# Performance work log

Measured on AMD Instinct MI355X. Metric: run time of the kernel, lower is better.

The kernel has to match this reference:

```python
import jax, jax.numpy as jnp
import numpy as np

SCORE_THR = 0.01
IOU_THR = 0.1          # NOTE: original layer hardcodes 0.1 in tf.image.non_max_suppression
MAX_DET = 100
NEG = jnp.float32(-1e30)


def _iou_one_vs_all(box, boxes):
    # box: [4] (y1,x1,y2,x2), boxes: [N,4]
    y1 = jnp.maximum(box[0], boxes[:, 0])
    x1 = jnp.maximum(box[1], boxes[:, 1])
    y2 = jnp.minimum(box[2], boxes[:, 2])
    x2 = jnp.minimum(box[3], boxes[:, 3])
    inter = jnp.maximum(y2 - y1, 0.0) * jnp.maximum(x2 - x1, 0.0)
    a = (box[2] - box[0]) * (box[3] - box[1])
    b = (boxes[:, 2] - boxes[:, 0]) * (boxes[:, 3] - boxes[:, 1])
    return inter / (a + b - inter + 1e-8)


def _nms_keep(boxes, scores):
    # Greedy NMS as a keep-mask over N anchors. Matches tf.image.non_max_suppression
    # restricted to anchors with score > SCORE_THR, up to MAX_DET selections.
    s = jnp.where(scores > SCORE_THR, scores, NEG)
    keep0 = jnp.zeros(s.shape, dtype=bool)

    def step(carry, _):
        s, keep = carry
        i = jnp.argmax(s)
        ok = s[i] > NEG * 0.5
        keep = keep.at[i].set(ok)
        iou = _iou_one_vs_all(boxes[i], boxes)
        s = jnp.where((iou > IOU_THR) & ok, NEG, s)
        s = s.at[i].set(NEG)
        return (s, keep), None

    (_, keep), _ = jax.lax.scan(step, (s, keep0), None, length=MAX_DET)
    return keep


def _filter_image(boxes_i, cls_i):
    # boxes_i: [N,4], cls_i: [N,C]
    C = cls_i.shape[1]
    # class-specific NMS: keep mask per class -> [C, N]
    keep = jax.vmap(lambda s: _nms_keep(boxes_i, s))(cls_i.T)
    keep_flat = keep.T.reshape(-1)          # [N*C], (anchor, class) flat order
    flat = cls_i.reshape(-1)                # [N*C]
    masked = jnp.where(keep_flat, flat, NEG)
    vals, idx = jax.lax.top_k(masked, MAX_DET)
    valid = vals > NEG * 0.5
    anchor = idx // C
    label = idx % C
    scores_out = jnp.where(valid, jnp.take(flat, idx), -1.0)
    boxes_out = jnp.where(valid[:, None], boxes_i[anchor], -1.0)
    labels_out = jnp.where(valid, label, -1).astype(jnp.int32)
    return boxes_out, scores_out, labels_out


def setup_inputs() -> dict:
    key = jax.random.key(0)
    k1, k2, k3 = jax.random.split(key, 3)
    B, N, C = 4, 49104, 90
    yx1 = jax.random.uniform(k1, (B, N, 2), dtype=jnp.float32) * 512.0
    hw = jax.random.uniform(k2, (B, N, 2), dtype=jnp.float32) * 128.0 + 1.0
    boxes = jnp.concatenate([yx1, yx1 + hw], axis=-1)          # [B,N,4] y1x1y2x2
    classification = jax.random.uniform(k3, (B, N, C), dtype=jnp.float32)
    return {"boxes": boxes, "classification": classification}


def reference(boxes, classification):
    return jax.vmap(_filter_image)(boxes, classification)
```

## Files before the change

kernel.cpp:

```cpp
#include <hip/hip_runtime.h>
#include <stdint.h>

typedef unsigned long long u64;

#define B_ 4
#define N_ 49104
#define C_ 90
#define NCLS (B_ * C_)
#define MAXK 100
#define THR 0.01f
#define NBH 288
#define BINLO 1760
#define KCAP 640
#define PTGT 448
#define PCAP 512
#define ACH 128
#define NCH ((N_ + ACH - 1) / ACH)
#define CAPC 32
#define NBIN_M 1280
#define BINBASE 0x3F6E0000u
#define BINSH_M 10
#define T0 0.99f

__device__ __forceinline__ float area_of(float y1, float x1, float y2, float x2) {
#pragma clang fp contract(off)
  return (y2 - y1) * (x2 - x1);
}

#define IOU_MID (26843547.0 / 268435456.0)

__device__ __forceinline__ bool iou_gt(float ay1, float ax1, float ay2, float ax2, float aa,
                                       float by1, float bx1, float by2, float bx2, float ba) {
#pragma clang fp contract(off)
  float y1 = fmaxf(ay1, by1);
  float x1 = fmaxf(ax1, bx1);
  float y2 = fminf(ay2, by2);
  float x2 = fminf(ax2, bx2);
  float inter = fmaxf(y2 - y1, 0.0f) * fmaxf(x2 - x1, 0.0f);
  float denom = aa + ba - inter + 1e-8f;
  return (double)inter >= IOU_MID * (double)denom;
}

__device__ __forceinline__ u64 umax64(u64 a, u64 b) { return a > b ? a : b; }

__device__ __forceinline__ u64 shfl_xor_u64(u64 v, int m) {
  int lo = __shfl_xor((int)(unsigned)v, m);
  int hi = __shfl_xor((int)(unsigned)(v >> 32), m);
  return ((u64)(unsigned)hi << 32) | (u64)(unsigned)lo;
}

__device__ __forceinline__ int key2bin_m(u64 k) {
  int d = (int)((unsigned)(k >> 32) - BINBASE);
  int bin = d >> BINSH_M;
  if (d < 0) bin = 0;
  if (bin > NBIN_M - 1) bin = NBIN_M - 1;
  return bin;
}

__device__ __forceinline__ int keybin_h(u64 k) {
  int bin = (int)((unsigned)(k >> 44) & 2047) - BINLO;
  if (bin < 0) bin = 0;
  if (bin > NBH - 1) bin = NBH - 1;
  return bin;
}

__global__ __launch_bounds__(256) void select_kernel(const float* __restrict__ cls,
                                                     u64* __restrict__ keybuf,
                                                     unsigned* __restrict__ cnt,
                                                     int capsel, float t0) {
  __shared__ u64 ll[C_ * CAPC];
  __shared__ unsigned lcnt[C_];
  __shared__ unsigned base_s[C_];
  int blk = blockIdx.x;
  int b = blk / NCH, ch = blk - b * NCH;
  int a0 = ch * ACH;
  int aEnd = a0 + ACH; if (aEnd > N_) aEnd = N_;
  int e0 = a0 * C_;
  int nelem = (aEnd - a0) * C_;
  int tid = threadIdx.x;

  for (int i = tid; i < C_; i += 256) lcnt[i] = 0u;
  __syncthreads();

  const float4* src4 = (const float4*)(cls + (size_t)b * N_ * C_ + e0);
  int n4 = nelem >> 2;
  for (int i4 = tid; i4 < n4; i4 += 256) {
    float4 v = src4[i4];
#pragma unroll
    for (int j = 0; j < 4; ++j) {
      float s = (&v.x)[j];
      if (s > t0) {
        int e = e0 + i4 * 4 + j;
        unsigned n = (unsigned)e / (unsigned)C_;
        unsigned c = (unsigned)e - n * (unsigned)C_;
        u64 key = ((u64)__float_as_uint(s) << 32) | (u64)(0xFFFFFFFFu - n);
        unsigned pos = atomicAdd(&lcnt[c], 1u);
        if (pos < CAPC) {
          ll[c * CAPC + pos] = key;
        } else {
          unsigned g = (unsigned)(b * C_) + c;
          unsigned gp = atomicAdd(&cnt[g * 16], 1u);
          if (gp < (unsigned)capsel) keybuf[(size_t)g * capsel + gp] = key;
        }
      }
    }
  }
  __syncthreads();

  if (tid < C_) {
    unsigned cc = lcnt[tid]; if (cc > CAPC) cc = CAPC;
    base_s[tid] = atomicAdd(&cnt[(b * C_ + tid) * 16], cc);
  }
  __syncthreads();

  for (int i = tid; i < C_ * CAPC; i += 256) {
    int c = i >> 5, j = i & 31;
    unsigned cc = lcnt[c]; if (cc > CAPC) cc = CAPC;
    if ((unsigned)j < cc) {
      unsigned pos = base_s[c] + (unsigned)j;
      if (pos < (unsigned)capsel)
        keybuf[(size_t)(b * C_ + c) * capsel + pos] = ll[i];
    }
  }
}

__global__ __launch_bounds__(512) void nms_kernel(const float* __restrict__ boxes,
                                                  const float* __restrict__ cls,
                                                  const u64* __restrict__ keybuf,
                                                  const unsigned* __restrict__ cnt,
                                                  unsigned* __restrict__ done,
                                                  int capsel, float t0,
                                                  u64* __restrict__ keepkeys,
                                                  int* __restrict__ nk_arr,
                                                  float* __restrict__ out) {
  int gcls = blockIdx.x;
  int b = gcls / C_, c = gcls - b * C_;
  __shared__ u64 karr[KCAP];
  __shared__ unsigned hist[NBH];
  __shared__ unsigned sfx[NBH];
  __shared__ unsigned histm[NBIN_M];
  __shared__ unsigned sfxm[NBIN_M];
  __shared__ float4 kb[MAXK];
  __shared__ float ka[MAXK];
  __shared__ unsigned wsum[8];
  __shared__ int sh_cnt[8];
  __shared__ int sh_b1, sh_run, sh_over;
  __shared__ int sh_last, sh_thr;
  __shared__ unsigned sh_cc;
  int tid = threadIdx.x;
  int lane = tid & 63;
  int wid = tid >> 6;

  for (int i = tid; i < MAXK; i += 512) keepkeys[(size_t)gcls * MAXK + i] = 0ull;
  for (int i = tid; i < NBH; i += 512) hist[i] = 0u;
  if (tid == 0) sh_over = 0;
  __syncthreads();

  unsigned Mraw = cnt[gcls * 16];
  bool overflow = (Mraw > (unsigned)capsel);
  int M = overflow ? 0 : (int)Mraw;

  const u64* src = keybuf + (size_t)gcls * capsel;

  const int PK = 4096 / 512;
  u64 kreg[PK];
#pragma unroll
  for (int q = 0; q < PK; ++q) {
    kreg[q] = 0ull;
    int i = q * 512 + tid;
    if (i < M) {
      kreg[q] = src[i];
      atomicAdd(&hist[keybin_h(kreg[q])], 1u);
    }
  }
  __syncthreads();

  {
    unsigned psum = (tid < NBH) ? hist[NBH - 1 - tid] : 0u;
    unsigned incl = psum;
#pragma unroll
    for (int s = 1; s < 64; s <<= 1) {
      unsigned v = (unsigned)__shfl_up((int)incl, s);
      if (lane >= s) incl += v;
    }
    if (lane == 63 && wid < 5) wsum[wid] = incl;
    __syncthreads();
    if (tid < NBH) {
      unsigned base2 = 0;
      for (int w2 = 0; w2 < wid; ++w2) base2 += wsum[w2];
      sfx[NBH - 1 - tid] = base2 + incl;
    }
  }
  __syncthreads();

  const float4* bx4 = (const float4*)(boxes + (size_t)b * N_ * 4);

  int seen = 0;
  int ext = 0;
  int bhi = NBH;
  while (ext < M && seen < MAXK) {
    if (tid == 0) sh_b1 = -1;
    __syncthreads();
    int rem = M - ext;
    int target = rem < PTGT ? rem : PTGT;
    {
      int mymax = -1;
      if (tid < NBH && tid < bhi && (int)sfx[tid] >= ext + target) mymax = tid;
      for (int m = 32; m > 0; m >>= 1) {
        int o = __shfl_xor(mymax, m);
        mymax = o > mymax ? o : mymax;
      }
      if (lane == 0 && mymax >= 0) atomicMax(&sh_b1, mymax);
    }
    __syncthreads();
    if (tid == 0) {
      int b1 = sh_b1;
      int run = (int)sfx[b1] - ext;
      int blo = b1;
      if (run > PCAP) {
        blo = b1 + 1;
        run = (blo < NBH) ? (int)sfx[blo] - ext : 0;
      }
      if (run == 0) sh_over = 1;
      sh_b1 = blo; sh_run = run;
    }
    __syncthreads();
    if (sh_over) break;
    int blo = sh_b1, run = sh_run;

#pragma unroll
    for (int q = 0; q < PK; ++q) {
      int i = q * 512 + tid;
      if (i < M) {
        u64 k = kreg[q];
        int bin = keybin_h(k);
        if (bin >= blo && bin < bhi) {
          unsigned old = atomicSub(&hist[bin], 1u);
          karr[(int)sfx[bin] - (int)old - ext] = k;
        }
      }
    }
    __syncthreads();

    {
      u64 mk2 = 0ull; int mt = -1;
      if (tid < run) {
        u64 k = karr[tid];
        int bin = keybin_h(k);
        int hi2 = (int)sfx[bin] - ext;
        int lo2 = (bin >= NBH - 1) ? 0 : ((int)sfx[bin + 1] - ext);
        if (lo2 < 0) lo2 = 0;
        int r = lo2;
        for (int j = lo2; j < hi2; ++j) r += (karr[j] > k);
        mk2 = k; mt = r;
      }
      __syncthreads();
      if (mt >= 0) karr[mt] = mk2;
    }
    __syncthreads();

    {
      bool have = tid < run;
      float4 cb = make_float4(0.f, 0.f, 0.f, 0.f);
      float ca = 0.f;
      if (have) {
        u64 k = karr[tid];
        cb = bx4[0xFFFFFFFFu - (unsigned)(k & 0xFFFFFFFFull)];
        ca = area_of(cb.x, cb.y, cb.z, cb.w);
      }
      bool dead = !have;
      for (int j = 0; j < seen; ++j) {
        float4 sb = kb[j]; float sa = ka[j];
        dead |= iou_gt(sb.x, sb.y, sb.z, sb.w, sa,
                       cb.x, cb.y, cb.z, cb.w, ca);
      }
      u64 alive = __ballot(!dead);

      int nslice = (run + 63) >> 6;
      for (int s = 0; s < nslice; ++s) {
        if (wid == s) {
          int nkl = seen;
          int slo = s << 6;
          while (alive != 0ull && nkl < MAXK) {
            int bit = __ffsll((long long)alive) - 1;
            float sy1 = __shfl(cb.x, bit);
            float sx1 = __shfl(cb.y, bit);
            float sy2 = __shfl(cb.z, bit);
            float sx2 = __shfl(cb.w, bit);
            float sa  = __shfl(ca,   bit);
            if (lane == 0) {
              u64 key = karr[slo + bit];
              unsigned anchor = 0xFFFFFFFFu - (unsigned)(key & 0xFFFFFFFFull);
              unsigned flat = anchor * C_ + (unsigned)c;
              keepkeys[(size_t)gcls * MAXK + nkl] =
                  (key & 0xFFFFFFFF00000000ull) | (u64)(0xFFFFFFFFu - flat);
              kb[nkl] = make_float4(sy1, sx1, sy2, sx2);
              ka[nkl] = sa;
            }
            ++nkl;
            alive &= ~__ballot(iou_gt(sy1, sx1, sy2, sx2, sa,
                                      cb.x, cb.y, cb.z, cb.w, ca));
          }
          if (lane == 0) sh_cnt[s] = nkl;
          seen = nkl;
        }
        __syncthreads();
        int nkNew = (wid == s) ? seen : sh_cnt[s];
        if (nkNew >= MAXK) { seen = nkNew; break; }
        if (wid > s && nkNew > seen) {
          bool d2 = false;
          for (int j = seen; j < nkNew; ++j) {
            float4 sb = kb[j]; float sa = ka[j];
            d2 |= iou_gt(sb.x, sb.y, sb.z, sb.w, sa,
                         cb.x, cb.y, cb.z, cb.w, ca);
          }
          alive &= __ballot(!d2);
        }
        seen = nkNew;
      }
    }
    ext += run;
    bhi = blo;
    __syncthreads();
  }

  int nkF = seen;
  if (nkF < MAXK) {
    float teff;
    if (overflow)      teff = 2.0f;
    else if (sh_over)  teff = __uint_as_float(0x3F000000u | ((((unsigned)(bhi + BINLO)) << 12) - 1u));
    else               teff = t0;
    const float* sbase = cls + (size_t)b * N_ * C_ + c;
    const float* bx = boxes + (size_t)b * N_ * 4;
    u64* kkp = keepkeys + (size_t)gcls * MAXK;
    u64* red = karr;
    int nk2 = nkF;
    while (nk2 < MAXK) {
      u64 best = 0ull;
      for (int n = tid; n < N_; n += 512) {
        float s = sbase[(size_t)n * C_];
        if (s > THR && s <= teff) {
          float y1 = bx[(size_t)n * 4 + 0], x1 = bx[(size_t)n * 4 + 1];
          float y2 = bx[(size_t)n * 4 + 2], x2 = bx[(size_t)n * 4 + 3];
          float ar = area_of(y1, x1, y2, x2);
          bool ov = false;
          for (int j = 0; j < nk2; ++j) {
            float4 kbj = kb[j];
            if (iou_gt(kbj.x, kbj.y, kbj.z, kbj.w, ka[j], y1, x1, y2, x2, ar)) { ov = true; break; }
          }
          if (!ov) {
            u64 key = ((u64)__float_as_uint(s) << 32) | (u64)(0xFFFFFFFFu - (unsigned)n);
            best = umax64(best, key);
          }
        }
      }
      red[tid] = best;
      __syncthreads();
      for (int sft = 256; sft > 0; sft >>= 1) {
        if (tid < sft) red[tid] = umax64(red[tid], red[tid + sft]);
        __syncthreads();
      }
      u64 sel = red[0];
      __syncthreads();
      if (sel == 0ull) {
        if (tid == 0) {
          unsigned target2 = 0xFFFFFFFFu - (unsigned)c;
          for (int j = 0; j < nk2; ++j)
            if ((unsigned)(kkp[j] & 0xFFFFFFFFull) == target2) kkp[j] = 0ull;
        }
        break;
      }
      unsigned anchor = 0xFFFFFFFFu - (unsigned)(sel & 0xFFFFFFFFull);
      if (tid == 0) {
        float y1 = bx[(size_t)anchor * 4 + 0], x1 = bx[(size_t)anchor * 4 + 1];
        float y2 = bx[(size_t)anchor * 4 + 2], x2 = bx[(size_t)anchor * 4 + 3];
        kb[nk2] = make_float4(y1, x1, y2, x2);
        ka[nk2] = area_of(y1, x1, y2, x2);
        unsigned flat = anchor * C_ + (unsigned)c;
        kkp[nk2] = (sel & 0xFFFFFFFF00000000ull) | (u64)(0xFFFFFFFFu - flat);
      }
      ++nk2;
      __syncthreads();
    }
    nkF = nk2;
  }
  if (tid == 0) nk_arr[gcls] = nkF;

  __syncthreads();
  if (tid == 0) {
    __threadfence();
    sh_last = (atomicAdd(&done[b], 1u) == (unsigned)(C_ - 1)) ? 1 : 0;
  }
  __syncthreads();
  if (!sh_last) return;
  __threadfence();

  {
    const u64* kk = keepkeys + (size_t)b * C_ * MAXK;
    const int TOT = C_ * MAXK;
    u64* mk = karr;
    u64* selk = karr + 512;

    for (int i = tid; i < NBIN_M; i += 512) histm[i] = 0u;
    for (int r = tid; r < MAXK; r += 512) selk[r] = 0ull;
    if (tid == 0) { sh_thr = -1; sh_cc = 0u; }
    __syncthreads();
    for (int i = tid; i < TOT; i += 512) {
      u64 k = kk[i];
      if (k != 0ull) atomicAdd(&histm[key2bin_m(k)], 1u);
    }
    __syncthreads();

    const int Wm = 3;
    int j0 = tid * Wm;
    unsigned psum = 0;
#pragma unroll
    for (int q = 0; q < Wm; ++q) {
      int bin = NBIN_M - 1 - (j0 + q);
      if (bin >= 0) psum += histm[bin];
    }
    unsigned incl = psum;
#pragma unroll
    for (int s = 1; s < 64; s <<= 1) {
      unsigned v = (unsigned)__shfl_up((int)incl, s);
      if (lane >= s) incl += v;
    }
    if (lane == 63) wsum[wid] = incl;
    __syncthreads();
    unsigned base = incl - psum;
    for (int w2 = 0; w2 < wid; ++w2) base += wsum[w2];
    unsigned running = base;
    int mythr = -1;
#pragma unroll
    for (int q = 0; q < Wm; ++q) {
      int bin = NBIN_M - 1 - (j0 + q);
      if (bin >= 0) {
        running += histm[bin];
        sfxm[bin] = running;
        if (mythr < 0 && running >= (unsigned)MAXK) mythr = bin;
      }
    }
    if (mythr >= 0) atomicMax(&sh_thr, mythr);
    __syncthreads();

    int thr = sh_thr; if (thr < 0) thr = 0;
    unsigned S = sfxm[thr];

    if (S <= 512u) {
      for (int i = tid; i < TOT; i += 512) {
        u64 k = kk[i];
        if (k != 0ull && key2bin_m(k) >= thr) {
          unsigned pos = atomicAdd(&sh_cc, 1u);
          mk[pos] = k;
        }
      }
      __syncthreads();
      u64 myk = (tid < (int)S) ? mk[tid] : 0ull;
      int r = 0;
      for (int j = 0; j < (int)S; ++j) r += (mk[j] > myk);
      __syncthreads();
      if (tid < (int)S && r < MAXK) selk[r] = myk;
      __syncthreads();
    } else {
      if (wid == 0) {
        int c0 = lane, c1 = lane + 64;
        int len0 = (c0 < C_) ? nk_arr[b * C_ + c0] : 0;
        int len1 = (c1 < C_) ? nk_arr[b * C_ + c1] : 0;
        int h0 = 0, h1 = 0;
        auto fetchc = [&](int cc, int& h, int len) -> u64 {
          while (h < len) {
            u64 k = kk[(size_t)cc * MAXK + h];
            if (k != 0ull) return k;
            ++h;
          }
          return 0ull;
        };
        u64 cand0 = (c0 < C_) ? fetchc(c0, h0, len0) : 0ull;
        u64 cand1 = (c1 < C_) ? fetchc(c1, h1, len1) : 0ull;
        for (int r2 = 0; r2 < MAXK; ++r2) {
          u64 my = umax64(cand0, cand1);
          u64 g = my;
#pragma unroll
          for (int m = 1; m < 64; m <<= 1) g = umax64(g, shfl_xor_u64(g, m));
          if (lane == 0) selk[r2] = g;
          if (g != 0ull && my == g) {
            if (cand0 == g) { ++h0; cand0 = fetchc(c0, h0, len0); }
            else            { ++h1; cand1 = fetchc(c1, h1, len1); }
          }
        }
      }
      __syncthreads();
    }

    for (int r2 = tid; r2 < MAXK; r2 += 512) {
      u64 s = selk[r2];
      float oy1, ox1, oy2, ox2, sc, lb;
      if (s != 0ull) {
        unsigned flat = 0xFFFFFFFFu - (unsigned)(s & 0xFFFFFFFFull);
        unsigned anchor = flat / C_;
        unsigned label = flat - anchor * C_;
        sc = __uint_as_float((unsigned)(s >> 32));
        const float4 bp = ((const float4*)(boxes + (size_t)b * N_ * 4))[anchor];
        oy1 = bp.x; ox1 = bp.y; oy2 = bp.z; ox2 = bp.w;
        lb = (float)label;
      } else {
        oy1 = ox1 = oy2 = ox2 = -1.0f; sc = -1.0f; lb = -1.0f;
      }
      float* bo = out + ((size_t)b * MAXK + r2) * 4;
      bo[0] = oy1; bo[1] = ox1; bo[2] = oy2; bo[3] = ox2;
      out[(size_t)B_ * MAXK * 4 + b * MAXK + r2] = sc;
      out[(size_t)B_ * MAXK * 4 + B_ * MAXK + b * MAXK + r2] = lb;
    }
  }
}

extern "C" void kernel_launch(void* const* d_in, const int* in_sizes, int n_in,
                              void* d_out, int out_size, void* d_ws, size_t ws_size,
                              hipStream_t stream) {
  const float* boxes = (const float*)d_in[0];
  const float* cls = (const float*)d_in[1];
  char* ws = (char*)d_ws;

  int capsel;
  auto need_for = [](int cap) -> size_t {
    return 23104 + (size_t)NCLS * cap * 8 + 288000 + 1440;
  };
  if (ws_size >= need_for(4096))      capsel = 4096;
  else if (ws_size >= need_for(2048)) capsel = 2048;
  else                                capsel = 1024;

  unsigned* cnt = (unsigned*)ws;
  unsigned* done = (unsigned*)(ws + 23040);
  u64* keybuf = (u64*)(ws + 23104);
  size_t off = 23104 + (size_t)NCLS * capsel * 8;
  u64* keepkeys = (u64*)(ws + off);      off += 288000;
  int* nk_arr = (int*)(ws + off);

  hipMemsetAsync(ws, 0, 23104, stream);
  select_kernel<<<B_ * NCH, 256, 0, stream>>>(cls, keybuf, cnt, capsel, T0);
  nms_kernel<<<NCLS, 512, 0, stream>>>(boxes, cls, keybuf, cnt, done, capsel, T0,
                                       keepkeys, nk_arr, (float*)d_out);
}
```

Baseline: 170.6 us.

## Build merge histogram per class block and scan only kept keys per class

Each per-class NMS block now adds its kept keys into a per-image global histogram using atomics, so the last block loads that histogram instead of rescanning all 9000 key slots. The candidate-gather pass now walks each class's kept list, which is in descending score order, up to its length and stops at the first key below the threshold bin. This takes serial work off the tail block that runs after all classes finish, in exchange for global atomics from every block and a larger memset.

```diff
diff --git a/kernel.cpp b/kernel.cpp
--- a/kernel.cpp
+++ b/kernel.cpp
@@ -129,6 +129,7 @@
                                                   const u64* __restrict__ keybuf,
                                                   const unsigned* __restrict__ cnt,
                                                   unsigned* __restrict__ done,
+                                                  unsigned* __restrict__ mhist,
                                                   int capsel, float t0,
                                                   u64* __restrict__ keepkeys,
                                                   int* __restrict__ nk_arr,
@@ -142,6 +143,7 @@
   __shared__ unsigned sfxm[NBIN_M];
   __shared__ float4 kb[MAXK];
   __shared__ float ka[MAXK];
+  __shared__ u64 kkey_lds[MAXK];
   __shared__ unsigned wsum[8];
   __shared__ int sh_cnt[8];
   __shared__ int sh_b1, sh_run, sh_over;
@@ -151,7 +153,10 @@
   int lane = tid & 63;
   int wid = tid >> 6;
 
-  for (int i = tid; i < MAXK; i += 512) keepkeys[(size_t)gcls * MAXK + i] = 0ull;
+  for (int i = tid; i < MAXK; i += 512) {
+    keepkeys[(size_t)gcls * MAXK + i] = 0ull;
+    kkey_lds[i] = 0ull;
+  }
   for (int i = tid; i < NBH; i += 512) hist[i] = 0u;
   if (tid == 0) sh_over = 0;
   __syncthreads();
@@ -292,8 +297,9 @@
               u64 key = karr[slo + bit];
               unsigned anchor = 0xFFFFFFFFu - (unsigned)(key & 0xFFFFFFFFull);
               unsigned flat = anchor * C_ + (unsigned)c;
-              keepkeys[(size_t)gcls * MAXK + nkl] =
-                  (key & 0xFFFFFFFF00000000ull) | (u64)(0xFFFFFFFFu - flat);
+              u64 kk2 = (key & 0xFFFFFFFF00000000ull) | (u64)(0xFFFFFFFFu - flat);
+              keepkeys[(size_t)gcls * MAXK + nkl] = kk2;
+              kkey_lds[nkl] = kk2;
               kb[nkl] = make_float4(sy1, sx1, sy2, sx2);
               ka[nkl] = sa;
             }
@@ -366,7 +372,7 @@
         if (tid == 0) {
           unsigned target2 = 0xFFFFFFFFu - (unsigned)c;
           for (int j = 0; j < nk2; ++j)
-            if ((unsigned)(kkp[j] & 0xFFFFFFFFull) == target2) kkp[j] = 0ull;
+            if ((unsigned)(kkp[j] & 0xFFFFFFFFull) == target2) { kkp[j] = 0ull; kkey_lds[j] = 0ull; }
         }
         break;
       }
@@ -377,7 +383,9 @@
         kb[nk2] = make_float4(y1, x1, y2, x2);
         ka[nk2] = area_of(y1, x1, y2, x2);
         unsigned flat = anchor * C_ + (unsigned)c;
-        kkp[nk2] = (sel & 0xFFFFFFFF00000000ull) | (u64)(0xFFFFFFFFu - flat);
+        u64 kk2 = (sel & 0xFFFFFFFF00000000ull) | (u64)(0xFFFFFFFFu - flat);
+        kkp[nk2] = kk2;
+        kkey_lds[nk2] = kk2;
       }
       ++nk2;
       __syncthreads();
@@ -385,8 +393,14 @@
     nkF = nk2;
   }
   if (tid == 0) nk_arr[gcls] = nkF;
-
-  __syncthreads();
+  __syncthreads();
+
+  for (int i = tid; i < nkF; i += 512) {
+    u64 k = kkey_lds[i];
+    if (k != 0ull) atomicAdd(&mhist[b * NBIN_M + key2bin_m(k)], 1u);
+  }
+  __syncthreads();
+
   if (tid == 0) {
     __threadfence();
     sh_last = (atomicAdd(&done[b], 1u) == (unsigned)(C_ - 1)) ? 1 : 0;
@@ -397,18 +411,12 @@
 
   {
     const u64* kk = keepkeys + (size_t)b * C_ * MAXK;
-    const int TOT = C_ * MAXK;
     u64* mk = karr;
     u64* selk = karr + 512;
 
-    for (int i = tid; i < NBIN_M; i += 512) histm[i] = 0u;
+    for (int i = tid; i < NBIN_M; i += 512) histm[i] = mhist[b * NBIN_M + i];
     for (int r = tid; r < MAXK; r += 512) selk[r] = 0ull;
     if (tid == 0) { sh_thr = -1; sh_cc = 0u; }
-    __syncthreads();
-    for (int i = tid; i < TOT; i += 512) {
-      u64 k = kk[i];
-      if (k != 0ull) atomicAdd(&histm[key2bin_m(k)], 1u);
-    }
     __syncthreads();
 
     const int Wm = 3;
@@ -447,9 +455,13 @@
     unsigned S = sfxm[thr];
 
     if (S <= 512u) {
-      for (int i = tid; i < TOT; i += 512) {
-        u64 k = kk[i];
-        if (k != 0ull && key2bin_m(k) >= thr) {
+      if (tid < C_) {
+        int lenc = nk_arr[b * C_ + tid];
+        const u64* kc = kk + (size_t)tid * MAXK;
+        for (int h = 0; h < lenc; ++h) {
+          u64 k = kc[h];
+          if (k == 0ull) continue;
+          if (key2bin_m(k) < thr) break;
           unsigned pos = atomicAdd(&sh_cc, 1u);
           mk[pos] = k;
         }
@@ -523,7 +535,7 @@
 
   int capsel;
   auto need_for = [](int cap) -> size_t {
-    return 23104 + (size_t)NCLS * cap * 8 + 288000 + 1440;
+    return 43584 + (size_t)NCLS * cap * 8 + 288000 + 1440;
   };
   if (ws_size >= need_for(4096))      capsel = 4096;
   else if (ws_size >= need_for(2048)) capsel = 2048;
@@ -531,13 +543,14 @@
 
   unsigned* cnt = (unsigned*)ws;
   unsigned* done = (unsigned*)(ws + 23040);
-  u64* keybuf = (u64*)(ws + 23104);
-  size_t off = 23104 + (size_t)NCLS * capsel * 8;
+  unsigned* mhist = (unsigned*)(ws + 23104);
+  u64* keybuf = (u64*)(ws + 43584);
+  size_t off = 43584 + (size_t)NCLS * capsel * 8;
   u64* keepkeys = (u64*)(ws + off);      off += 288000;
   int* nk_arr = (int*)(ws + off);
 
-  hipMemsetAsync(ws, 0, 23104, stream);
+  hipMemsetAsync(ws, 0, 43584, stream);
   select_kernel<<<B_ * NCH, 256, 0, stream>>>(cls, keybuf, cnt, capsel, T0);
-  nms_kernel<<<NCLS, 512, 0, stream>>>(boxes, cls, keybuf, cnt, done, capsel, T0,
+  nms_kernel<<<NCLS, 512, 0, stream>>>(boxes, cls, keybuf, cnt, done, mhist, capsel, T0,
                                        keepkeys, nk_arr, (float*)d_out);
 }
```

Result: slower. 181.3 us (+6.3%).
